# Performance work log

Hardware: AMD Instinct MI355X
Metric: run time of the kernel (lower is better)

## Reference

```python
import jax, jax.numpy as jnp
import numpy as np

D_MODEL = 512
NHEAD = 8
D_K = D_MODEL // NHEAD
SCALE = float(np.sqrt(D_K))


def setup_inputs() -> dict:
    key = jax.random.key(0)
    ks = jax.random.split(key, 11)
    B, S = 2, 4096
    std = 1.0 / np.sqrt(D_MODEL)
    inp = {
        'q': jax.random.normal(ks[0], (B, S, D_MODEL), jnp.float32),
        'k': jax.random.normal(ks[1], (B, S, D_MODEL), jnp.float32),
        'v': jax.random.normal(ks[2], (B, S, D_MODEL), jnp.float32),
        'w_q': jax.random.normal(ks[3], (D_MODEL, D_MODEL), jnp.float32) * std,
        'b_q': jax.random.normal(ks[4], (D_MODEL,), jnp.float32) * std,
        'w_k': jax.random.normal(ks[5], (D_MODEL, D_MODEL), jnp.float32) * std,
        'b_k': jax.random.normal(ks[6], (D_MODEL,), jnp.float32) * std,
        'w_v': jax.random.normal(ks[7], (D_MODEL, D_MODEL), jnp.float32) * std,
        'b_v': jax.random.normal(ks[8], (D_MODEL,), jnp.float32) * std,
        'w_o': jax.random.normal(ks[9], (D_MODEL, D_MODEL), jnp.float32) * std,
        'b_o': jax.random.normal(ks[10], (D_MODEL,), jnp.float32) * std,
    }
    return inp


def reference(q, k, v, w_q, b_q, w_k, b_k, w_v, b_v, w_o, b_o):
    B, S, _ = q.shape
    # torch Linear: y = x @ W.T + b
    def proj(x, W, b):
        y = x @ W.T + b
        return y.reshape(B, -1, NHEAD, D_K).transpose(0, 2, 1, 3)  # [B,H,S,Dk]
    qh = proj(q, w_q, b_q)
    kh = proj(k, w_k, b_k)
    vh = proj(v, w_v, b_v)
    scores = jnp.einsum('bhsd,bhtd->bhst', qh, kh) / SCALE  # [B,H,S,S]
    attn = jax.nn.softmax(scores, axis=-1)
    out = jnp.einsum('bhst,bhtd->bhsd', attn, vh)  # [B,H,S,Dk]
    out = out.transpose(0, 2, 1, 3).reshape(B, S, D_MODEL)
    return out @ w_o.T + b_o
```

## Files before the change

kernel.cpp:

```cpp
#include <hip/hip_runtime.h>
#include <stdint.h>

#define DM 512
#define S_LEN 4096
#define NH 8
#define DK 64

typedef __attribute__((ext_vector_type(8))) short bf16x8;
typedef __attribute__((ext_vector_type(4))) float f32x4;

#define QSCALE 0.18033688011112042f
#define NEGBIAS -17.312340490667562f

__device__ inline ushort f2bf(float f) {
  union { float f; uint32_t u; } v; v.f = f;
  uint32_t r = v.u + 0x7fff + ((v.u >> 16) & 1);
  return (ushort)(r >> 16);
}
__device__ inline uint32_t fu(float f) {
  union { float f; uint32_t u; } v; v.f = f; return v.u;
}
__device__ inline uint32_t pktrunc(float lo, float hi) {
  return __builtin_amdgcn_perm(fu(hi), fu(lo), 0x07060302);
}

__device__ inline void async_cp16(const ushort* g, ushort* l) {
  __builtin_amdgcn_global_load_lds((const __attribute__((address_space(1))) void*)g,
                                   (__attribute__((address_space(3))) void*)l, 16, 0, 0);
}

__global__ __launch_bounds__(256) void cvt_w(const float4* __restrict__ s0, ushort* __restrict__ d0,
                                             const float4* __restrict__ s1, ushort* __restrict__ d1,
                                             const float4* __restrict__ s2, ushort* __restrict__ d2,
                                             const float4* __restrict__ s3, ushort* __restrict__ d3) {
  int i = blockIdx.x * 256 + threadIdx.x;
  {
    float4 v = s0[i];
    ushort4 o = {f2bf(v.x), f2bf(v.y), f2bf(v.z), f2bf(v.w)};
    *(ushort4*)&d0[i * 4] = o;
  }
  {
    float4 v = s1[i];
    ushort4 o = {f2bf(v.x), f2bf(v.y), f2bf(v.z), f2bf(v.w)};
    *(ushort4*)&d1[i * 4] = o;
  }
  {
    float4 v = s2[i];
    ushort4 o = {f2bf(v.x), f2bf(v.y), f2bf(v.z), f2bf(v.w)};
    *(ushort4*)&d2[i * 4] = o;
  }
  {
    float4 v = s3[i];
    ushort4 o = {f2bf(v.x), f2bf(v.y), f2bf(v.z), f2bf(v.w)};
    *(ushort4*)&d3[i * 4] = o;
  }
}

__global__ __launch_bounds__(256) void gemm_proj(
    const float* __restrict__ q, const float* __restrict__ k, const float* __restrict__ v,
    const ushort* __restrict__ wq, const ushort* __restrict__ wk, const ushort* __restrict__ wv,
    const float* __restrict__ bq, const float* __restrict__ bk, const float* __restrict__ bv,
    ushort* __restrict__ Qh, ushort* __restrict__ Kh, ushort* __restrict__ VhT) {
  const float* A; const ushort* Bt; const float* bias; float cs;
  if (blockIdx.z == 0)      { A = q; Bt = wq; bias = bq; cs = QSCALE; }
  else if (blockIdx.z == 1) { A = k; Bt = wk; bias = bk; cs = 1.0f; }
  else                      { A = v; Bt = wv; bias = bv; cs = 1.0f; }

  __shared__ ushort As[128 * 32];
  __shared__ ushort Bs[128 * 32];
  const int tid = threadIdx.x;
  const int w = tid >> 6, lane = tid & 63;
  const int quad = lane >> 4, l16 = lane & 15;
  const int wm = w >> 1, wn = w & 1;
  const int m0 = blockIdx.y * 128, n0 = blockIdx.x * 128;
  const f32x4 zero4 = {0.f, 0.f, 0.f, 0.f};

  f32x4 acc[4][4];
  #pragma unroll
  for (int i = 0; i < 4; i++)
    #pragma unroll
    for (int j = 0; j < 4; j++) acc[i][j] = zero4;

  for (int kb = 0; kb < 16; kb++) {
    const int k0 = kb * 32;
    #pragma unroll
    for (int r = 0; r < 2; r++) {
      int idx = r * 256 + tid;
      async_cp16(&Bt[(size_t)(n0 + (idx >> 2)) * DM + k0 + (idx & 3) * 8], &Bs[idx * 8]);
    }
    #pragma unroll
    for (int r = 0; r < 2; r++) {
      int idx = r * 256 + tid;
      int row = idx >> 2, col = (idx & 3) * 8;
      const float* src = &A[(size_t)(m0 + row) * DM + k0 + col];
      float4 a0 = *(const float4*)src;
      float4 a1 = *(const float4*)(src + 4);
      uint2 w0 = {pktrunc(a0.x, a0.y), pktrunc(a0.z, a0.w)};
      uint2 w1 = {pktrunc(a1.x, a1.y), pktrunc(a1.z, a1.w)};
      *(uint2*)&As[row * 32 + col] = w0;
      *(uint2*)&As[row * 32 + col + 4] = w1;
    }
    __syncthreads();
    bf16x8 af[4], bfr[4];
    #pragma unroll
    for (int i = 0; i < 4; i++) {
      af[i]  = *(const bf16x8*)&As[(wm * 64 + i * 16 + l16) * 32 + quad * 8];
      bfr[i] = *(const bf16x8*)&Bs[(wn * 64 + i * 16 + l16) * 32 + quad * 8];
    }
    #pragma unroll
    for (int i = 0; i < 4; i++)
      #pragma unroll
      for (int j = 0; j < 4; j++)
        acc[i][j] = __builtin_amdgcn_mfma_f32_16x16x32_bf16(af[i], bfr[j], acc[i][j], 0, 0, 0);
    __syncthreads();
  }

  if (blockIdx.z != 2) {
    ushort* C = (blockIdx.z == 0) ? Qh : Kh;
    #pragma unroll
    for (int j = 0; j < 4; j++) {
      int col_g = n0 + wn * 64 + j * 16 + l16;
      float bv = bias[col_g];
      int h = col_g >> 6, d = col_g & 63;
      #pragma unroll
      for (int i = 0; i < 4; i++) {
        #pragma unroll
        for (int r = 0; r < 4; r++) {
          int row_g = m0 + wm * 64 + i * 16 + quad * 4 + r;
          int b = row_g >> 12, s = row_g & 4095;
          C[(((size_t)(b * NH + h) << 12) + s) * DK + d] = f2bf((acc[i][j][r] + bv) * cs);
        }
      }
    }
  } else {
    #pragma unroll
    for (int j = 0; j < 4; j++) {
      int col_g = n0 + wn * 64 + j * 16 + l16;
      float bv = bias[col_g];
      int h = col_g >> 6, d = col_g & 63;
      #pragma unroll
      for (int i = 0; i < 4; i++) {
        int row0 = m0 + wm * 64 + i * 16 + quad * 4;
        int b = row0 >> 12, s0 = row0 & 4095;
        int sl = s0 & 31;
        int sp = (s0 & ~31) | (((sl >> 2) & 3) << 3) | (((sl >> 4) & 1) << 2);
        ushort4 pk = {f2bf(acc[i][j][0] + bv), f2bf(acc[i][j][1] + bv),
                      f2bf(acc[i][j][2] + bv), f2bf(acc[i][j][3] + bv)};
        *(ushort4*)&VhT[((size_t)(b * NH + h) * DK + d) * S_LEN + sp] = pk;
      }
    }
  }
}

__global__ __launch_bounds__(256) void gemm_out(const ushort* __restrict__ A,
                                                const ushort* __restrict__ Bt,
                                                const float* __restrict__ bias,
                                                float* __restrict__ C) {
  __shared__ ushort As[128 * 32];
  __shared__ ushort Bs[128 * 32];
  const int tid = threadIdx.x;
  const int w = tid >> 6, lane = tid & 63;
  const int quad = lane >> 4, l16 = lane & 15;
  const int wm = w >> 1, wn = w & 1;
  const int m0 = blockIdx.y * 128, n0 = blockIdx.x * 128;
  const f32x4 zero4 = {0.f, 0.f, 0.f, 0.f};

  f32x4 acc[4][4];
  #pragma unroll
  for (int i = 0; i < 4; i++)
    #pragma unroll
    for (int j = 0; j < 4; j++) acc[i][j] = zero4;

  for (int kb = 0; kb < 16; kb++) {
    const int k0 = kb * 32;
    #pragma unroll
    for (int r = 0; r < 2; r++) {
      int idx = r * 256 + tid;
      async_cp16(&A [(size_t)(m0 + (idx >> 2)) * DM + k0 + (idx & 3) * 8], &As[idx * 8]);
      async_cp16(&Bt[(size_t)(n0 + (idx >> 2)) * DM + k0 + (idx & 3) * 8], &Bs[idx * 8]);
    }
    __syncthreads();
    bf16x8 af[4], bfr[4];
    #pragma unroll
    for (int i = 0; i < 4; i++) {
      af[i]  = *(const bf16x8*)&As[(wm * 64 + i * 16 + l16) * 32 + quad * 8];
      bfr[i] = *(const bf16x8*)&Bs[(wn * 64 + i * 16 + l16) * 32 + quad * 8];
    }
    #pragma unroll
    for (int i = 0; i < 4; i++)
      #pragma unroll
      for (int j = 0; j < 4; j++)
        acc[i][j] = __builtin_amdgcn_mfma_f32_16x16x32_bf16(af[i], bfr[j], acc[i][j], 0, 0, 0);
    __syncthreads();
  }

  #pragma unroll
  for (int j = 0; j < 4; j++) {
    int col_g = n0 + wn * 64 + j * 16 + l16;
    float bv = bias[col_g];
    #pragma unroll
    for (int i = 0; i < 4; i++) {
      #pragma unroll
      for (int r = 0; r < 4; r++) {
        int row_g = m0 + wm * 64 + i * 16 + quad * 4 + r;
        C[(size_t)row_g * DM + col_g] = acc[i][j][r] + bv;
      }
    }
  }
}

__global__ __launch_bounds__(256, 2) void attn(const ushort* __restrict__ Qh,
                                               const ushort* __restrict__ Kh,
                                               const ushort* __restrict__ VhT,
                                               ushort* __restrict__ O) {
  __shared__ ushort Ks[2][128 * 64];
  __shared__ ushort Vt[2][64 * 128];
  const int tid = threadIdx.x;
  const int w = tid >> 6, lane = tid & 63;
  const int quad = lane >> 4, l16 = lane & 15;
  const int bh = blockIdx.x;
  const int q0 = blockIdx.y * 128 + w * 32;
  const size_t base = (size_t)bh * S_LEN * DK;
  const f32x4 zero4 = {0.f, 0.f, 0.f, 0.f};
  const f32x4 negb = {NEGBIAS, NEGBIAS, NEGBIAS, NEGBIAS};
  const short one_bf = (short)0x3F80;
  const bf16x8 ones = {one_bf, one_bf, one_bf, one_bf, one_bf, one_bf, one_bf, one_bf};

  bf16x8 qf[2][2];
  #pragma unroll
  for (int i = 0; i < 2; i++)
    #pragma unroll
    for (int c = 0; c < 2; c++)
      qf[i][c] = *(const bf16x8*)&Qh[base + (size_t)(q0 + i * 16 + l16) * DK + c * 32 + quad * 8];

  f32x4 o[2][4];
  f32x4 l_acc[2];
  #pragma unroll
  for (int i = 0; i < 2; i++) {
    l_acc[i] = zero4;
    #pragma unroll
    for (int n = 0; n < 4; n++) o[i][n] = zero4;
  }

  #define STAGE(IT, BUF) do {                                                       \
    const int t0_ = (IT) * 128;                                                     \
    _Pragma("unroll")                                                               \
    for (int r_ = 0; r_ < 4; r_++) {                                                \
      int idx = r_ * 256 + tid;                                                     \
      int row = idx >> 3;                                                           \
      int cl = ((idx & 7) << 4) ^ ((row & 7) << 4);                                 \
      async_cp16(&Kh[base + (size_t)(t0_ + row) * DK + (cl >> 1)], &Ks[BUF][idx * 8]); \
    }                                                                               \
    _Pragma("unroll")                                                               \
    for (int r_ = 0; r_ < 4; r_++) {                                                \
      int idx = r_ * 256 + tid;                                                     \
      int row = idx >> 4;                                                           \
      int cl = ((idx & 15) << 4) ^ ((row & 7) << 4);                                \
      async_cp16(&VhT[base + (size_t)row * S_LEN + t0_ + (cl >> 1)], &Vt[BUF][idx * 8]); \
    }                                                                               \
  } while (0)

  STAGE(0, 0);
  __syncthreads();

  const int swz = (l16 & 7) << 4;

  for (int it = 0; it < 32; it++) {
    const int cur = it & 1;
    if (it < 31) STAGE(it + 1, cur ^ 1);
    const ushort* Kb = &Ks[cur][0];
    const ushort* Vb = &Vt[cur][0];

    #pragma unroll
    for (int half = 0; half < 2; half++) {
      bf16x8 kf[4][2];
      #pragma unroll
      for (int s = 0; s < 4; s++) {
        int row = half * 64 + s * 16 + l16;
        kf[s][0] = *(const bf16x8*)&Kb[row * 64 + ((( 0 + quad * 16) ^ swz) >> 1)];
        kf[s][1] = *(const bf16x8*)&Kb[row * 64 + (((64 + quad * 16) ^ swz) >> 1)];
      }
      f32x4 sc[2][4];
      __builtin_amdgcn_s_setprio(1);
      #pragma unroll
      for (int i = 0; i < 2; i++)
        #pragma unroll
        for (int s = 0; s < 4; s++) {
          f32x4 t = negb;
          t = __builtin_amdgcn_mfma_f32_16x16x32_bf16(kf[s][0], qf[i][0], t, 0, 0, 0);
          t = __builtin_amdgcn_mfma_f32_16x16x32_bf16(kf[s][1], qf[i][1], t, 0, 0, 0);
          sc[i][s] = t;
        }
      __builtin_amdgcn_s_setprio(0);
      float p[2][4][4];
      #pragma unroll
      for (int i = 0; i < 2; i++)
        #pragma unroll
        for (int s = 0; s < 4; s++)
          #pragma unroll
          for (int r = 0; r < 4; r++)
            p[i][s][r] = __builtin_amdgcn_exp2f(sc[i][s][r]);
      union { bf16x8 v; uint32_t u[4]; } pf[2][2];
      #pragma unroll
      for (int i = 0; i < 2; i++)
        #pragma unroll
        for (int ppl = 0; ppl < 2; ppl++) {
          int s0 = ppl * 2, s1 = ppl * 2 + 1;
          pf[i][ppl].u[0] = pktrunc(p[i][s0][0], p[i][s0][1]);
          pf[i][ppl].u[1] = pktrunc(p[i][s0][2], p[i][s0][3]);
          pf[i][ppl].u[2] = pktrunc(p[i][s1][0], p[i][s1][1]);
          pf[i][ppl].u[3] = pktrunc(p[i][s1][2], p[i][s1][3]);
          l_acc[i] = __builtin_amdgcn_mfma_f32_16x16x32_bf16(pf[i][ppl].v, ones, l_acc[i], 0, 0, 0);
        }
      bf16x8 vf[4][2];
      #pragma unroll
      for (int n = 0; n < 4; n++) {
        int row = n * 16 + l16;
        #pragma unroll
        for (int ppl = 0; ppl < 2; ppl++)
          vf[n][ppl] = *(const bf16x8*)&Vb[row * 128 + ((((half * 2 + ppl) * 64 + quad * 16) ^ swz) >> 1)];
      }
      __builtin_amdgcn_s_setprio(1);
      #pragma unroll
      for (int n = 0; n < 4; n++)
        #pragma unroll
        for (int ppl = 0; ppl < 2; ppl++)
          #pragma unroll
          for (int i = 0; i < 2; i++)
            o[i][n] = __builtin_amdgcn_mfma_f32_16x16x32_bf16(pf[i][ppl].v, vf[n][ppl], o[i][n], 0, 0, 0);
      __builtin_amdgcn_s_setprio(0);
    }
    __syncthreads();
  }

  const int b = bh >> 3, h = bh & 7;
  #pragma unroll
  for (int i = 0; i < 2; i++) {
    #pragma unroll
    for (int r = 0; r < 4; r++) {
      float inv = 1.0f / l_acc[i][r];
      int qq = q0 + i * 16 + quad * 4 + r;
      #pragma unroll
      for (int n = 0; n < 4; n++) {
        int d = n * 16 + l16;
        O[(size_t)(b * S_LEN + qq) * DM + h * DK + d] = f2bf(o[i][n][r] * inv);
      }
    }
  }
}

extern "C" void kernel_launch(void* const* d_in, const int* in_sizes, int n_in,
                              void* d_out, int out_size, void* d_ws, size_t ws_size,
                              hipStream_t stream) {
  const float* q   = (const float*)d_in[0];
  const float* k   = (const float*)d_in[1];
  const float* v   = (const float*)d_in[2];
  const float* w_q = (const float*)d_in[3];
  const float* b_q = (const float*)d_in[4];
  const float* w_k = (const float*)d_in[5];
  const float* b_k = (const float*)d_in[6];
  const float* w_v = (const float*)d_in[7];
  const float* b_v = (const float*)d_in[8];
  const float* w_o = (const float*)d_in[9];
  const float* b_o = (const float*)d_in[10];

  const size_t W_ELEMS = (size_t)DM * DM;
  const size_t HEADS_ELEMS = (size_t)2 * NH * S_LEN * DK;
  ushort* wqb = (ushort*)d_ws;
  ushort* wkb = wqb + W_ELEMS;
  ushort* wvb = wkb + W_ELEMS;
  ushort* wob = wvb + W_ELEMS;
  ushort* Qh  = wob + W_ELEMS;
  ushort* Kh  = Qh + HEADS_ELEMS;
  ushort* VhT = Kh + HEADS_ELEMS;
  ushort* AttO = VhT + HEADS_ELEMS;

  cvt_w<<<256, 256, 0, stream>>>((const float4*)w_q, wqb, (const float4*)w_k, wkb,
                                 (const float4*)w_v, wvb, (const float4*)w_o, wob);
  gemm_proj<<<dim3(4, 64, 3), 256, 0, stream>>>(q, k, v, wqb, wkb, wvb,
                                                b_q, b_k, b_v, Qh, Kh, VhT);
  attn<<<dim3(16, 32), 256, 0, stream>>>(Qh, Kh, VhT, AttO);
  gemm_out<<<dim3(4, 64), 256, 0, stream>>>(AttO, wob, b_o, (float*)d_out);
}
```

Measured before the change: 226.2 us.

## Split attention KV tile across two wave groups with shared-memory reduction

The attention block grows from 256 to 512 threads. Each group of four waves now handles one 64-key half of every 128-key tile, where before each wave looped over both halves. Partial O and row-sum accumulators from the second group are combined through LDS at the end. The goal is more waves per CU to hide MFMA, exp and LDS latency, at the cost of an extra reduction pass and higher register and occupancy pressure from launch_bounds(512,4).

```diff
diff --git a/kernel.cpp b/kernel.cpp
--- a/kernel.cpp
+++ b/kernel.cpp
@@ -209,17 +209,18 @@
   }
 }
 
-__global__ __launch_bounds__(256, 2) void attn(const ushort* __restrict__ Qh,
+__global__ __launch_bounds__(512, 4) void attn(const ushort* __restrict__ Qh,
                                                const ushort* __restrict__ Kh,
                                                const ushort* __restrict__ VhT,
                                                ushort* __restrict__ O) {
-  __shared__ ushort Ks[2][128 * 64];
-  __shared__ ushort Vt[2][64 * 128];
+  __shared__ ushort smem[2][16384];
   const int tid = threadIdx.x;
   const int w = tid >> 6, lane = tid & 63;
   const int quad = lane >> 4, l16 = lane & 15;
+  const int half = w >> 2;
+  const int qw = w & 3;
   const int bh = blockIdx.x;
-  const int q0 = blockIdx.y * 128 + w * 32;
+  const int q0 = blockIdx.y * 128 + qw * 32;
   const size_t base = (size_t)bh * S_LEN * DK;
   const f32x4 zero4 = {0.f, 0.f, 0.f, 0.f};
   const f32x4 negb = {NEGBIAS, NEGBIAS, NEGBIAS, NEGBIAS};
@@ -242,22 +243,22 @@
     for (int n = 0; n < 4; n++) o[i][n] = zero4;
   }
 
-  #define STAGE(IT, BUF) do {                                                       \
-    const int t0_ = (IT) * 128;                                                     \
-    _Pragma("unroll")                                                               \
-    for (int r_ = 0; r_ < 4; r_++) {                                                \
-      int idx = r_ * 256 + tid;                                                     \
-      int row = idx >> 3;                                                           \
-      int cl = ((idx & 7) << 4) ^ ((row & 7) << 4);                                 \
-      async_cp16(&Kh[base + (size_t)(t0_ + row) * DK + (cl >> 1)], &Ks[BUF][idx * 8]); \
-    }                                                                               \
-    _Pragma("unroll")                                                               \
-    for (int r_ = 0; r_ < 4; r_++) {                                                \
-      int idx = r_ * 256 + tid;                                                     \
-      int row = idx >> 4;                                                           \
-      int cl = ((idx & 15) << 4) ^ ((row & 7) << 4);                                \
-      async_cp16(&VhT[base + (size_t)row * S_LEN + t0_ + (cl >> 1)], &Vt[BUF][idx * 8]); \
-    }                                                                               \
+  #define STAGE(IT, BUF) do {                                                         \
+    const int t0_ = (IT) * 128;                                                       \
+    _Pragma("unroll")                                                                 \
+    for (int r_ = 0; r_ < 2; r_++) {                                                  \
+      int idx = r_ * 512 + tid;                                                       \
+      int row = idx >> 3;                                                             \
+      int cl = ((idx & 7) << 4) ^ ((row & 7) << 4);                                   \
+      async_cp16(&Kh[base + (size_t)(t0_ + row) * DK + (cl >> 1)], &smem[BUF][idx * 8]); \
+    }                                                                                 \
+    _Pragma("unroll")                                                                 \
+    for (int r_ = 0; r_ < 2; r_++) {                                                  \
+      int idx = r_ * 512 + tid;                                                       \
+      int row = idx >> 4;                                                             \
+      int cl = ((idx & 15) << 4) ^ ((row & 7) << 4);                                  \
+      async_cp16(&VhT[base + (size_t)row * S_LEN + t0_ + (cl >> 1)], &smem[BUF][8192 + idx * 8]); \
+    }                                                                                 \
   } while (0)
 
   STAGE(0, 0);
@@ -268,82 +269,101 @@
   for (int it = 0; it < 32; it++) {
     const int cur = it & 1;
     if (it < 31) STAGE(it + 1, cur ^ 1);
-    const ushort* Kb = &Ks[cur][0];
-    const ushort* Vb = &Vt[cur][0];
-
-    #pragma unroll
-    for (int half = 0; half < 2; half++) {
-      bf16x8 kf[4][2];
+    const ushort* Kb = &smem[cur][0];
+    const ushort* Vb = &smem[cur][8192];
+
+    bf16x8 kf[4][2];
+    #pragma unroll
+    for (int s = 0; s < 4; s++) {
+      int row = half * 64 + s * 16 + l16;
+      kf[s][0] = *(const bf16x8*)&Kb[row * 64 + ((( 0 + quad * 16) ^ swz) >> 1)];
+      kf[s][1] = *(const bf16x8*)&Kb[row * 64 + (((64 + quad * 16) ^ swz) >> 1)];
+    }
+    f32x4 sc[2][4];
+    __builtin_amdgcn_s_setprio(1);
+    #pragma unroll
+    for (int i = 0; i < 2; i++)
       #pragma unroll
       for (int s = 0; s < 4; s++) {
-        int row = half * 64 + s * 16 + l16;
-        kf[s][0] = *(const bf16x8*)&Kb[row * 64 + ((( 0 + quad * 16) ^ swz) >> 1)];
-        kf[s][1] = *(const bf16x8*)&Kb[row * 64 + (((64 + quad * 16) ^ swz) >> 1)];
-      }
-      f32x4 sc[2][4];
-      __builtin_amdgcn_s_setprio(1);
-      #pragma unroll
-      for (int i = 0; i < 2; i++)
+        f32x4 t = negb;
+        t = __builtin_amdgcn_mfma_f32_16x16x32_bf16(kf[s][0], qf[i][0], t, 0, 0, 0);
+        t = __builtin_amdgcn_mfma_f32_16x16x32_bf16(kf[s][1], qf[i][1], t, 0, 0, 0);
+        sc[i][s] = t;
+      }
+    __builtin_amdgcn_s_setprio(0);
+    float p[2][4][4];
+    #pragma unroll
+    for (int i = 0; i < 2; i++)
+      #pragma unroll
+      for (int s = 0; s < 4; s++)
         #pragma unroll
-        for (int s = 0; s < 4; s++) {
-          f32x4 t = negb;
-          t = __builtin_amdgcn_mfma_f32_16x16x32_bf16(kf[s][0], qf[i][0], t, 0, 0, 0);
-          t = __builtin_amdgcn_mfma_f32_16x16x32_bf16(kf[s][1], qf[i][1], t, 0, 0, 0);
-          sc[i][s] = t;
+        for (int r = 0; r < 4; r++)
+          p[i][s][r] = __builtin_amdgcn_exp2f(sc[i][s][r]);
+    union { bf16x8 v; uint32_t u[4]; } pf[2][2];
+    #pragma unroll
+    for (int i = 0; i < 2; i++)
+      #pragma unroll
+      for (int ppl = 0; ppl < 2; ppl++) {
+        int s0 = ppl * 2, s1 = ppl * 2 + 1;
+        pf[i][ppl].u[0] = pktrunc(p[i][s0][0], p[i][s0][1]);
+        pf[i][ppl].u[1] = pktrunc(p[i][s0][2], p[i][s0][3]);
+        pf[i][ppl].u[2] = pktrunc(p[i][s1][0], p[i][s1][1]);
+        pf[i][ppl].u[3] = pktrunc(p[i][s1][2], p[i][s1][3]);
+        l_acc[i] = __builtin_amdgcn_mfma_f32_16x16x32_bf16(pf[i][ppl].v, ones, l_acc[i], 0, 0, 0);
+      }
+    bf16x8 vf[4][2];
+    #pragma unroll
+    for (int n = 0; n < 4; n++) {
+      int row = n * 16 + l16;
+      #pragma unroll
+      for (int ppl = 0; ppl < 2; ppl++)
+        vf[n][ppl] = *(const bf16x8*)&Vb[row * 128 + ((((half * 2 + ppl) * 64 + quad * 16) ^ swz) >> 1)];
+    }
+    __builtin_amdgcn_s_setprio(1);
+    #pragma unroll
+    for (int n = 0; n < 4; n++)
+      #pragma unroll
+      for (int ppl = 0; ppl < 2; ppl++)
+        #pragma unroll
+        for (int i = 0; i < 2; i++)
+          o[i][n] = __builtin_amdgcn_mfma_f32_16x16x32_bf16(pf[i][ppl].v, vf[n][ppl], o[i][n], 0, 0, 0);
+    __builtin_amdgcn_s_setprio(0);
+
+    __syncthreads();
+  }
+
+  float* red = (float*)smem;
+  const int roff = (qw * 64 + lane) * 40;
+  if (half == 1) {
+    #pragma unroll
+    for (int i = 0; i < 2; i++) {
+      #pragma unroll
+      for (int n = 0; n < 4; n++)
+        *(f32x4*)&red[roff + (i * 4 + n) * 4] = o[i][n];
+      *(f32x4*)&red[roff + 32 + i * 4] = l_acc[i];
+    }
+  }
+  __syncthreads();
+  if (half == 0) {
+    #pragma unroll
+    for (int i = 0; i < 2; i++) {
+      #pragma unroll
+      for (int n = 0; n < 4; n++)
+        o[i][n] += *(const f32x4*)&red[roff + (i * 4 + n) * 4];
+      l_acc[i] += *(const f32x4*)&red[roff + 32 + i * 4];
+    }
+    const int b = bh >> 3, h = bh & 7;
+    #pragma unroll
+    for (int i = 0; i < 2; i++) {
+      #pragma unroll
+      for (int r = 0; r < 4; r++) {
+        float inv = 1.0f / l_acc[i][r];
+        int qq = q0 + i * 16 + quad * 4 + r;
+        #pragma unroll
+        for (int n = 0; n < 4; n++) {
+          int d = n * 16 + l16;
+          O[(size_t)(b * S_LEN + qq) * DM + h * DK + d] = f2bf(o[i][n][r] * inv);
         }
-      __builtin_amdgcn_s_setprio(0);
-      float p[2][4][4];
-      #pragma unroll
-      for (int i = 0; i < 2; i++)
-        #pragma unroll
-        for (int s = 0; s < 4; s++)
-          #pragma unroll
-          for (int r = 0; r < 4; r++)
-            p[i][s][r] = __builtin_amdgcn_exp2f(sc[i][s][r]);
-      union { bf16x8 v; uint32_t u[4]; } pf[2][2];
-      #pragma unroll
-      for (int i = 0; i < 2; i++)
-        #pragma unroll
-        for (int ppl = 0; ppl < 2; ppl++) {
-          int s0 = ppl * 2, s1 = ppl * 2 + 1;
-          pf[i][ppl].u[0] = pktrunc(p[i][s0][0], p[i][s0][1]);
-          pf[i][ppl].u[1] = pktrunc(p[i][s0][2], p[i][s0][3]);
-          pf[i][ppl].u[2] = pktrunc(p[i][s1][0], p[i][s1][1]);
-          pf[i][ppl].u[3] = pktrunc(p[i][s1][2], p[i][s1][3]);
-          l_acc[i] = __builtin_amdgcn_mfma_f32_16x16x32_bf16(pf[i][ppl].v, ones, l_acc[i], 0, 0, 0);
-        }
-      bf16x8 vf[4][2];
-      #pragma unroll
-      for (int n = 0; n < 4; n++) {
-        int row = n * 16 + l16;
-        #pragma unroll
-        for (int ppl = 0; ppl < 2; ppl++)
-          vf[n][ppl] = *(const bf16x8*)&Vb[row * 128 + ((((half * 2 + ppl) * 64 + quad * 16) ^ swz) >> 1)];
-      }
-      __builtin_amdgcn_s_setprio(1);
-      #pragma unroll
-      for (int n = 0; n < 4; n++)
-        #pragma unroll
-        for (int ppl = 0; ppl < 2; ppl++)
-          #pragma unroll
-          for (int i = 0; i < 2; i++)
-            o[i][n] = __builtin_amdgcn_mfma_f32_16x16x32_bf16(pf[i][ppl].v, vf[n][ppl], o[i][n], 0, 0, 0);
-      __builtin_amdgcn_s_setprio(0);
-    }
-    __syncthreads();
-  }
-
-  const int b = bh >> 3, h = bh & 7;
-  #pragma unroll
-  for (int i = 0; i < 2; i++) {
-    #pragma unroll
-    for (int r = 0; r < 4; r++) {
-      float inv = 1.0f / l_acc[i][r];
-      int qq = q0 + i * 16 + quad * 4 + r;
-      #pragma unroll
-      for (int n = 0; n < 4; n++) {
-        int d = n * 16 + l16;
-        O[(size_t)(b * S_LEN + qq) * DM + h * DK + d] = f2bf(o[i][n][r] * inv);
       }
     }
   }
@@ -379,6 +399,6 @@
                                  (const float4*)w_v, wvb, (const float4*)w_o, wob);
   gemm_proj<<<dim3(4, 64, 3), 256, 0, stream>>>(q, k, v, wqb, wkb, wvb,
                                                 b_q, b_k, b_v, Qh, Kh, VhT);
-  attn<<<dim3(16, 32), 256, 0, stream>>>(Qh, Kh, VhT, AttO);
+  attn<<<dim3(16, 32), 512, 0, stream>>>(Qh, Kh, VhT, AttO);
   gemm_out<<<dim3(4, 64), 256, 0, stream>>>(AttO, wob, b_o, (float*)d_out);
 }
```

Measured after the change: 225.6 us. No clear change (-0.3%).
